# Kernel optimization log

Measured on AMD Instinct MI355X. Metric: run time of the kernel, lower is better.

## Reference

```python
import jax, jax.numpy as jnp
import numpy as np

BINS = 10
LOSS_WEIGHT = 1.0
N = 8388608


def setup_inputs() -> dict:
    key = jax.random.key(0)
    k1, k2 = jax.random.split(key)
    pred = jax.random.normal(k1, (N, 2), dtype=jnp.float32)
    target = jax.random.randint(k2, (N,), 0, 2, dtype=jnp.int64)
    return {"pred": pred, "target": target}


def reference(pred, target):
    # one-hot binary target, as in torch scatter_(1, target, 1) with class_num=2
    tgt = jax.nn.one_hot(target, 2, dtype=pred.dtype)  # [N, 2]
    # label_weight defaults to ones -> all elements valid
    tot = jnp.maximum(jnp.asarray(pred.size, pred.dtype), 1.0)

    # gradient magnitude g = |sigmoid(pred).detach() - target|, in [0, 1]
    g = jnp.abs(jax.nn.sigmoid(jax.lax.stop_gradient(pred)) - tgt)

    # edges are i/bins with edges[-1] += 1e-6, so bin = min(floor(g*bins), bins-1)
    bin_idx = jnp.clip((g * BINS).astype(jnp.int32), 0, BINS - 1)  # [N, 2]

    # histogram of valid samples per bin (all valid here)
    counts = jax.ops.segment_sum(
        jnp.ones((pred.size,), pred.dtype), bin_idx.reshape(-1), num_segments=BINS
    )  # [BINS]

    n_nonempty = (counts > 0).sum()
    per_bin_w = jnp.where(counts > 0, tot / jnp.maximum(counts, 1.0), 0.0)  # [BINS]
    weights = per_bin_w[bin_idx]  # [N, 2]
    weights = jnp.where(
        n_nonempty > 0, weights / n_nonempty.astype(pred.dtype), weights
    )
    weights = jax.lax.stop_gradient(weights)

    # stable BCE with logits: max(x,0) - x*t + log(1 + exp(-|x|))
    bce = jnp.maximum(pred, 0.0) - pred * tgt + jnp.log1p(jnp.exp(-jnp.abs(pred)))
    loss = jnp.sum(weights * bce) / tot
    return loss * LOSS_WEIGHT
```

## Files before the change

### kernel.cpp

```cpp
#include <hip/hip_runtime.h>

#define BINS 10
#define BLOCK 256
#define GRID 2048

#define LOG2E 1.44269504088896340736f
#define LN2   0.69314718055994530942f


__global__ void ghmc_init(double* ws) {
    int i = threadIdx.x;
    if (i < 2 * BINS) ws[i] = 0.0;
}

__device__ __forceinline__ void proc(float y, float2* __restrict__ hbase) {
    float a  = -fabsf(y) * LOG2E;
    float t  = __builtin_amdgcn_exp2f(a);
    float d  = 1.0f + t;
    float r  = __builtin_amdgcn_rcpf(d);
    float lg = __builtin_amdgcn_logf(d);
    float sp = fmaf(lg, LN2, fmaxf(y, 0.0f));
    float sg = (y >= 0.0f) ? r : t * r;
    int b = (int)(sg * 10.0f);
    b = b > (BINS - 1) ? (BINS - 1) : b;
    float2* h = hbase + (b << 8);
    float2 v = *h;
    v.x += 1.0f;
    v.y += sp;
    *h = v;
}

__device__ __forceinline__ void proc_row(float x0, float x1, int t,
                                         float2* __restrict__ hbase) {
    unsigned s0 = (unsigned)(t ^ 1) << 31;
    unsigned s1 = s0 ^ 0x80000000u;
    proc(__uint_as_float(__float_as_uint(x0) ^ s0), hbase);
    proc(__uint_as_float(__float_as_uint(x1) ^ s1), hbase);
}

template <int WRITE_MODE>
__global__ __launch_bounds__(BLOCK, 4) void ghmc_main(
    const float4* __restrict__ pred4,
    const int4*   __restrict__ tgt4,
    float2* __restrict__ partials,
    double* __restrict__ wsd,
    int nQuads, int nRows)
{
    __shared__ float2 hist[BINS][BLOCK];
    const int tid = threadIdx.x;
#pragma unroll
    for (int b = 0; b < BINS; ++b) hist[b][tid] = make_float2(0.f, 0.f);

    float2* hbase = &hist[0][tid];

    for (int i = blockIdx.x * BLOCK + tid; i < nQuads; i += GRID * BLOCK) {
        float4 pa = pred4[2 * i + 0];
        float4 pb = pred4[2 * i + 1];
        int4   tq = tgt4[i];
        proc_row(pa.x, pa.y, tq.x, hbase);
        proc_row(pa.z, pa.w, tq.y, hbase);
        proc_row(pb.x, pb.y, tq.z, hbase);
        proc_row(pb.z, pb.w, tq.w, hbase);
    }

    if (blockIdx.x == 0 && tid == 0) {
        const float* pf = (const float*)pred4;
        const int*   tf = (const int*)tgt4;
        for (int r = nQuads * 4; r < nRows; ++r)
            proc_row(pf[2 * r], pf[2 * r + 1], tf[r], hbase);
    }

    __syncthreads();

    if (tid < 128) {
#pragma unroll
        for (int b = 0; b < BINS; ++b) {
            float2 x = hist[b][tid], y = hist[b][tid + 128];
            hist[b][tid] = make_float2(x.x + y.x, x.y + y.y);
        }
    }
    __syncthreads();
    if (tid < 64) {
        float cx[BINS], cy[BINS];
#pragma unroll
        for (int b = 0; b < BINS; ++b) {
            float2 x = hist[b][tid], y = hist[b][tid + 64];
            cx[b] = x.x + y.x;
            cy[b] = x.y + y.y;
        }
#pragma unroll
        for (int off = 32; off > 0; off >>= 1) {
#pragma unroll
            for (int b = 0; b < BINS; ++b) {
                cx[b] += __shfl_down(cx[b], off, 64);
                cy[b] += __shfl_down(cy[b], off, 64);
            }
        }
        if (tid == 0) {
            if (WRITE_MODE == 0) {
#pragma unroll
                for (int b = 0; b < BINS; ++b)
                    partials[blockIdx.x * BINS + b] = make_float2(cx[b], cy[b]);
            } else {
#pragma unroll
                for (int b = 0; b < BINS; ++b) {
                    atomicAdd(&wsd[b],        (double)cx[b]);
                    atomicAdd(&wsd[BINS + b], (double)cy[b]);
                }
            }
        }
    }
}

__global__ __launch_bounds__(BLOCK) void ghmc_final_grid(
    const float2* __restrict__ partials, float* __restrict__ out, int nb)
{
    __shared__ double2 red[BINS][BLOCK];
    const int tid = threadIdx.x;
    double cx[BINS], cy[BINS];
#pragma unroll
    for (int b = 0; b < BINS; ++b) { cx[b] = 0.0; cy[b] = 0.0; }

    for (int p = tid; p < nb; p += BLOCK) {
#pragma unroll
        for (int b = 0; b < BINS; ++b) {
            float2 v = partials[p * BINS + b];
            cx[b] += (double)v.x;
            cy[b] += (double)v.y;
        }
    }
#pragma unroll
    for (int b = 0; b < BINS; ++b) red[b][tid] = make_double2(cx[b], cy[b]);
    __syncthreads();
    if (tid < 128) {
#pragma unroll
        for (int b = 0; b < BINS; ++b) {
            double2 x = red[b][tid], y = red[b][tid + 128];
            red[b][tid] = make_double2(x.x + y.x, x.y + y.y);
        }
    }
    __syncthreads();
    if (tid < 64) {
        double dx[BINS], dy[BINS];
#pragma unroll
        for (int b = 0; b < BINS; ++b) {
            double2 x = red[b][tid], y = red[b][tid + 64];
            dx[b] = x.x + y.x;
            dy[b] = x.y + y.y;
        }
#pragma unroll
        for (int off = 32; off > 0; off >>= 1) {
#pragma unroll
            for (int b = 0; b < BINS; ++b) {
                dx[b] += __shfl_down(dx[b], off, 64);
                dy[b] += __shfl_down(dy[b], off, 64);
            }
        }
        if (tid == 0) {
            int nz = 0;
            double acc = 0.0;
#pragma unroll
            for (int b = 0; b < BINS; ++b) {
                if (dx[b] > 0.0) { nz++; acc += dy[b] / dx[b]; }
            }
            out[0] = (float)((nz > 0) ? (acc / (double)nz) : 0.0);
        }
    }
}

__global__ void ghmc_final_atomic(const double* __restrict__ ws, float* __restrict__ out) {
    if (threadIdx.x == 0) {
        int nz = 0;
        double acc = 0.0;
#pragma unroll
        for (int b = 0; b < BINS; ++b) {
            double c = ws[b];
            if (c > 0.0) { nz++; acc += ws[BINS + b] / c; }
        }
        out[0] = (float)((nz > 0) ? (acc / (double)nz) : 0.0);
    }
}

extern "C" void kernel_launch(void* const* d_in, const int* in_sizes, int n_in,
                              void* d_out, int out_size, void* d_ws, size_t ws_size,
                              hipStream_t stream) {
    const float* pred = (const float*)d_in[0];
    const int* target = (const int*)d_in[1];
    const int nRows = in_sizes[1];
    const int nQuads = nRows / 4;
    float* out = (float*)d_out;

    const size_t need = (size_t)GRID * BINS * sizeof(float2);
    if (ws_size >= need) {
        float2* partials = (float2*)d_ws;
        ghmc_main<0><<<GRID, BLOCK, 0, stream>>>(
            (const float4*)pred, (const int4*)target, partials, nullptr, nQuads, nRows);
        ghmc_final_grid<<<1, BLOCK, 0, stream>>>(partials, out, GRID);
    } else {
        double* wsd = (double*)d_ws;
        ghmc_init<<<1, 64, 0, stream>>>(wsd);
        ghmc_main<1><<<GRID, BLOCK, 0, stream>>>(
            (const float4*)pred, (const int4*)target, nullptr, wsd, nQuads, nRows);
        ghmc_final_atomic<<<1, 64, 0, stream>>>(wsd, out);
    }
}
```

Measured before the change: 31.00 us.

## Simplify sigmoid/softplus math, split histograms per column, widen final reduction block

The per-element math now clamps the input and computes softplus and sigmoid straight from exp(y), which drops the abs, the select and the max. Each column of a row gets its own shared histogram, so back-to-back read-modify-writes no longer depend on each other. The final reduction block grows to 1024 threads and reduces per wave with shuffles before a small shared stage. The cost is double the LDS per block, which may limit occupancy under the launch bounds, plus a clamp that changes numerics for very large magnitudes.

```diff
diff --git a/kernel.cpp b/kernel.cpp
--- a/kernel.cpp
+++ b/kernel.cpp
@@ -14,13 +14,13 @@
 }
 
 __device__ __forceinline__ void proc(float y, float2* __restrict__ hbase) {
-    float a  = -fabsf(y) * LOG2E;
-    float t  = __builtin_amdgcn_exp2f(a);
-    float d  = 1.0f + t;
+    y = fminf(fmaxf(y, -80.0f), 80.0f);
+    float u  = __builtin_amdgcn_exp2f(y * LOG2E);
+    float d  = 1.0f + u;
     float r  = __builtin_amdgcn_rcpf(d);
     float lg = __builtin_amdgcn_logf(d);
-    float sp = fmaf(lg, LN2, fmaxf(y, 0.0f));
-    float sg = (y >= 0.0f) ? r : t * r;
+    float sg = u * r;
+    float sp = lg * LN2;
     int b = (int)(sg * 10.0f);
     b = b > (BINS - 1) ? (BINS - 1) : b;
     float2* h = hbase + (b << 8);
@@ -31,11 +31,12 @@
 }
 
 __device__ __forceinline__ void proc_row(float x0, float x1, int t,
-                                         float2* __restrict__ hbase) {
+                                         float2* __restrict__ hA,
+                                         float2* __restrict__ hB) {
     unsigned s0 = (unsigned)(t ^ 1) << 31;
     unsigned s1 = s0 ^ 0x80000000u;
-    proc(__uint_as_float(__float_as_uint(x0) ^ s0), hbase);
-    proc(__uint_as_float(__float_as_uint(x1) ^ s1), hbase);
+    proc(__uint_as_float(__float_as_uint(x0) ^ s0), hA);
+    proc(__uint_as_float(__float_as_uint(x1) ^ s1), hB);
 }
 
 template <int WRITE_MODE>
@@ -46,37 +47,47 @@
     double* __restrict__ wsd,
     int nQuads, int nRows)
 {
-    __shared__ float2 hist[BINS][BLOCK];
+    __shared__ float2 histA[BINS][BLOCK];
+    __shared__ float2 histB[BINS][BLOCK];
     const int tid = threadIdx.x;
 #pragma unroll
-    for (int b = 0; b < BINS; ++b) hist[b][tid] = make_float2(0.f, 0.f);
-
-    float2* hbase = &hist[0][tid];
+    for (int b = 0; b < BINS; ++b) {
+        histA[b][tid] = make_float2(0.f, 0.f);
+        histB[b][tid] = make_float2(0.f, 0.f);
+    }
+
+    float2* hA = &histA[0][tid];
+    float2* hB = &histB[0][tid];
 
     for (int i = blockIdx.x * BLOCK + tid; i < nQuads; i += GRID * BLOCK) {
         float4 pa = pred4[2 * i + 0];
         float4 pb = pred4[2 * i + 1];
         int4   tq = tgt4[i];
-        proc_row(pa.x, pa.y, tq.x, hbase);
-        proc_row(pa.z, pa.w, tq.y, hbase);
-        proc_row(pb.x, pb.y, tq.z, hbase);
-        proc_row(pb.z, pb.w, tq.w, hbase);
+        proc_row(pa.x, pa.y, tq.x, hA, hB);
+        proc_row(pa.z, pa.w, tq.y, hA, hB);
+        proc_row(pb.x, pb.y, tq.z, hA, hB);
+        proc_row(pb.z, pb.w, tq.w, hA, hB);
     }
 
     if (blockIdx.x == 0 && tid == 0) {
         const float* pf = (const float*)pred4;
         const int*   tf = (const int*)tgt4;
         for (int r = nQuads * 4; r < nRows; ++r)
-            proc_row(pf[2 * r], pf[2 * r + 1], tf[r], hbase);
-    }
-
+            proc_row(pf[2 * r], pf[2 * r + 1], tf[r], hA, hB);
+    }
+
+#pragma unroll
+    for (int b = 0; b < BINS; ++b) {
+        float2 a = histA[b][tid], c = histB[b][tid];
+        histA[b][tid] = make_float2(a.x + c.x, a.y + c.y);
+    }
     __syncthreads();
 
     if (tid < 128) {
 #pragma unroll
         for (int b = 0; b < BINS; ++b) {
-            float2 x = hist[b][tid], y = hist[b][tid + 128];
-            hist[b][tid] = make_float2(x.x + y.x, x.y + y.y);
+            float2 x = histA[b][tid], y = histA[b][tid + 128];
+            histA[b][tid] = make_float2(x.x + y.x, x.y + y.y);
         }
     }
     __syncthreads();
@@ -84,7 +95,7 @@
         float cx[BINS], cy[BINS];
 #pragma unroll
         for (int b = 0; b < BINS; ++b) {
-            float2 x = hist[b][tid], y = hist[b][tid + 64];
+            float2 x = histA[b][tid], y = histA[b][tid + 64];
             cx[b] = x.x + y.x;
             cy[b] = x.y + y.y;
         }
@@ -112,16 +123,17 @@
     }
 }
 
-__global__ __launch_bounds__(BLOCK) void ghmc_final_grid(
+__global__ __launch_bounds__(1024) void ghmc_final_grid(
     const float2* __restrict__ partials, float* __restrict__ out, int nb)
 {
-    __shared__ double2 red[BINS][BLOCK];
-    const int tid = threadIdx.x;
+    const int tid  = threadIdx.x;
+    const int wid  = tid >> 6;
+    const int lane = tid & 63;
     double cx[BINS], cy[BINS];
 #pragma unroll
     for (int b = 0; b < BINS; ++b) { cx[b] = 0.0; cy[b] = 0.0; }
 
-    for (int p = tid; p < nb; p += BLOCK) {
+    for (int p = tid; p < nb; p += 1024) {
 #pragma unroll
         for (int b = 0; b < BINS; ++b) {
             float2 v = partials[p * BINS + b];
@@ -130,41 +142,29 @@
         }
     }
 #pragma unroll
-    for (int b = 0; b < BINS; ++b) red[b][tid] = make_double2(cx[b], cy[b]);
+    for (int off = 32; off > 0; off >>= 1) {
+#pragma unroll
+        for (int b = 0; b < BINS; ++b) {
+            cx[b] += __shfl_down(cx[b], off, 64);
+            cy[b] += __shfl_down(cy[b], off, 64);
+        }
+    }
+    __shared__ double2 wred[16][BINS];
+    if (lane == 0) {
+#pragma unroll
+        for (int b = 0; b < BINS; ++b) wred[wid][b] = make_double2(cx[b], cy[b]);
+    }
     __syncthreads();
-    if (tid < 128) {
-#pragma unroll
-        for (int b = 0; b < BINS; ++b) {
-            double2 x = red[b][tid], y = red[b][tid + 128];
-            red[b][tid] = make_double2(x.x + y.x, x.y + y.y);
-        }
-    }
-    __syncthreads();
-    if (tid < 64) {
-        double dx[BINS], dy[BINS];
-#pragma unroll
-        for (int b = 0; b < BINS; ++b) {
-            double2 x = red[b][tid], y = red[b][tid + 64];
-            dx[b] = x.x + y.x;
-            dy[b] = x.y + y.y;
-        }
-#pragma unroll
-        for (int off = 32; off > 0; off >>= 1) {
-#pragma unroll
-            for (int b = 0; b < BINS; ++b) {
-                dx[b] += __shfl_down(dx[b], off, 64);
-                dy[b] += __shfl_down(dy[b], off, 64);
-            }
-        }
-        if (tid == 0) {
-            int nz = 0;
-            double acc = 0.0;
-#pragma unroll
-            for (int b = 0; b < BINS; ++b) {
-                if (dx[b] > 0.0) { nz++; acc += dy[b] / dx[b]; }
-            }
-            out[0] = (float)((nz > 0) ? (acc / (double)nz) : 0.0);
-        }
+    if (tid == 0) {
+        int nz = 0;
+        double acc = 0.0;
+#pragma unroll
+        for (int b = 0; b < BINS; ++b) {
+            double c = 0.0, s = 0.0;
+            for (int w = 0; w < 16; ++w) { c += wred[w][b].x; s += wred[w][b].y; }
+            if (c > 0.0) { nz++; acc += s / c; }
+        }
+        out[0] = (float)((nz > 0) ? (acc / (double)nz) : 0.0);
     }
 }
 
@@ -195,7 +195,7 @@
         float2* partials = (float2*)d_ws;
         ghmc_main<0><<<GRID, BLOCK, 0, stream>>>(
             (const float4*)pred, (const int4*)target, partials, nullptr, nQuads, nRows);
-        ghmc_final_grid<<<1, BLOCK, 0, stream>>>(partials, out, GRID);
+        ghmc_final_grid<<<1, 1024, 0, stream>>>(partials, out, GRID);
     } else {
         double* wsd = (double*)d_ws;
         ghmc_init<<<1, 64, 0, stream>>>(wsd);
```

After: 42.09 us. +35.8%, slower.
